# Kernel optimization log

Hardware: AMD Instinct MI355X
Metric: run time of the kernel (lower is better)

Reference implementation:

```python
import jax, jax.numpy as jnp
import numpy as np

N = 40000        # total gene nodes
E = 640000       # edges
F_IN = 128       # num_features
H = 128          # hidden_dim
SUB = 400        # genes per cell
EPS = 1e-5


def _bn(x, g, b):
    # BatchNorm1d, training-mode batch statistics (biased variance), deterministic
    m = x.mean(axis=0)
    v = x.var(axis=0)
    return (x - m) * jax.lax.rsqrt(v + EPS) * g + b


def _gcn_conv(x, W, b, src, dst):
    # PyG GCNConv: h = X W; add self-loops; symmetric deg^{-1/2} normalization;
    # scatter-add messages from src into dst; then add bias.
    h = x @ W                                   # [N, H]
    loop = jnp.arange(N)
    s = jnp.concatenate([src, loop])            # [E+N]
    d = jnp.concatenate([dst, loop])
    deg = jax.ops.segment_sum(jnp.ones(s.shape[0], h.dtype), d, num_segments=N)
    dis = jnp.where(deg > 0, deg ** -0.5, 0.0)  # deg_inv_sqrt
    norm = dis[s] * dis[d]                      # [E+N]
    out = jax.ops.segment_sum(h[s] * norm[:, None], d, num_segments=N)
    return out + b


def setup_inputs() -> dict:
    key = jax.random.key(0)
    ks = jax.random.split(key, 16)
    sc = lambda fan: 1.0 / np.sqrt(fan)
    inp = {
        "x": jax.random.normal(ks[0], (N, F_IN), jnp.float32),
        "edge_index": jax.random.randint(ks[1], (2, E), 0, N, jnp.int64),
        "conv1_w": jax.random.normal(ks[2], (F_IN, H), jnp.float32) * sc(F_IN),
        "conv1_b": jnp.zeros((H,), jnp.float32),
        "bn1_g": jnp.ones((H,), jnp.float32),
        "bn1_b": jnp.zeros((H,), jnp.float32),
        "conv2_w": jax.random.normal(ks[3], (H, H), jnp.float32) * sc(H),
        "conv2_b": jnp.zeros((H,), jnp.float32),
        "bn2_g": jnp.ones((H,), jnp.float32),
        "bn2_b": jnp.zeros((H,), jnp.float32),
        "att_w1": jax.random.normal(ks[4], (H, H // 2), jnp.float32) * sc(H),
        "att_b1": jnp.zeros((H // 2,), jnp.float32),
        "att_w2": jax.random.normal(ks[5], (H // 2, 1), jnp.float32) * sc(H // 2),
        "att_b2": jnp.zeros((1,), jnp.float32),
        "fc_w": jax.random.normal(ks[6], (H, H), jnp.float32) * sc(H),
        "fc_b": jnp.zeros((H,), jnp.float32),
        "bne_g": jnp.ones((H,), jnp.float32),
        "bne_b": jnp.zeros((H,), jnp.float32),
        "bot_w": jax.random.normal(ks[7], (H, 32), jnp.float32) * sc(H),
        "bot_b": jnp.zeros((32,), jnp.float32),
        "bnb_g": jnp.ones((32,), jnp.float32),
        "bnb_b": jnp.zeros((32,), jnp.float32),
    }
    return inp


def reference(x, edge_index, conv1_w, conv1_b, bn1_g, bn1_b,
              conv2_w, conv2_b, bn2_g, bn2_b,
              att_w1, att_b1, att_w2, att_b2,
              fc_w, fc_b, bne_g, bne_b,
              bot_w, bot_b, bnb_g, bnb_b):
    src, dst = edge_index[0], edge_index[1]
    # embed: two GCNConv + BN + ReLU (dropout omitted: deterministic reference)
    h = jax.nn.relu(_bn(_gcn_conv(x, conv1_w, conv1_b, src, dst), bn1_g, bn1_b))
    emb = jax.nn.relu(_bn(_gcn_conv(h, conv2_w, conv2_b, src, dst), bn2_g, bn2_b))
    # attention pooling over genes within each cell
    num_cells = N // SUB
    xr = emb.reshape(num_cells, SUB, H)                      # [C, S, H]
    scores = jnp.tanh(xr @ att_w1 + att_b1) @ att_w2 + att_b2  # [C, S, 1]
    w = jax.nn.softmax(scores, axis=1)
    pooled = jnp.sum(xr * w, axis=1)                          # [C, H]
    # dense head
    y = jax.nn.relu(_bn(pooled @ fc_w + fc_b, bne_g, bne_b))
    y = jax.nn.relu(_bn(y @ bot_w + bot_b, bnb_g, bnb_b))     # [C, 32]
    return (y, emb)
```

## Files before the change

### kernel.cpp

```cpp
#include <hip/hip_runtime.h>
#include <math.h>

typedef unsigned int u32;
typedef __attribute__((ext_vector_type(8))) short bf16x8;
typedef __attribute__((ext_vector_type(4))) float f32x4;

#define NN   40000
#define EE   640000
#define SUBG 400
#define CELLS 100
#define BNEPS 1e-5f
#define GB    2048
#define GEMMB 625
#define DEGB  512
#define FILLB 1024
#define SCALEB 2500

__device__ __forceinline__ u32 bf16pair(float a, float b) {
    u32 ua = __float_as_uint(a), ub = __float_as_uint(b);
    ua += 0x7fffu + ((ua >> 16) & 1u);
    ub += 0x7fffu + ((ub >> 16) & 1u);
    return (ua >> 16) | (ub & 0xffff0000u);
}
__device__ __forceinline__ float bflo(u32 u) { return __uint_as_float(u << 16); }
__device__ __forceinline__ float bfhi(u32 u) { return __uint_as_float(u & 0xffff0000u); }

__global__ void k_init(int* deg_cursor, const float* W1, u32* Wt1,
                       const float* W2, u32* Wt2, const float* wa, u32* Wta,
                       float* hstats) {
    int i = blockIdx.x * 256 + threadIdx.x;
    if (i < 2 * NN) { deg_cursor[i] = 0; return; }
    i -= 2 * NN;
    if (i < 16384) {
        const float* W = (i < 8192) ? W1 : W2;
        u32* Wt = (i < 8192) ? Wt1 : Wt2;
        int j = i & 8191;
        int n = j >> 6, k2 = (j & 63) * 2;
        Wt[n * 64 + (j & 63)] = bf16pair(W[k2 * 128 + n], W[(k2 + 1) * 128 + n]);
        return;
    }
    i -= 16384;
    if (i < 4096) {
        int n = i >> 6, k2 = (i & 63) * 2;
        Wta[n * 64 + (i & 63)] = bf16pair(wa[k2 * 64 + n], wa[(k2 + 1) * 64 + n]);
        return;
    }
    i -= 4096;
    if (i < 320) hstats[i] = 0.f;
}

__global__ __launch_bounds__(256)
void k_gemmdeg(const float* __restrict__ X, const u32* __restrict__ Wt,
               u32* __restrict__ Yb, const int* __restrict__ dst,
               int* __restrict__ deg) {
    int bid = blockIdx.x;
    int t = threadIdx.x;
    if (bid >= GEMMB) {
        int i = (bid - GEMMB) * 256 + t;
        int stride = DEGB * 256;
        for (; i < EE; i += stride) atomicAdd(&deg[dst[i]], 1);
        return;
    }
    int l = t & 63, wv = t >> 6;
    int rowbase = bid * 64 + wv * 16;
    int ml = l & 15, kg = l >> 4;

    f32x4 acc[8];
#pragma unroll
    for (int nt = 0; nt < 8; ++nt) acc[nt] = (f32x4){0.f, 0.f, 0.f, 0.f};
    const float* xr = X + (long)(rowbase + ml) * 128;
#pragma unroll
    for (int kk = 0; kk < 4; ++kk) {
        int k0 = kk * 32 + kg * 8;
        float4 xa = *(const float4*)&xr[k0];
        float4 xb = *(const float4*)&xr[k0 + 4];
        union { u32 u[4]; bf16x8 v; } af;
        af.u[0] = bf16pair(xa.x, xa.y);
        af.u[1] = bf16pair(xa.z, xa.w);
        af.u[2] = bf16pair(xb.x, xb.y);
        af.u[3] = bf16pair(xb.z, xb.w);
#pragma unroll
        for (int nt = 0; nt < 8; ++nt) {
            bf16x8 b = *(const bf16x8*)&Wt[(nt * 16 + ml) * 64 + (k0 >> 1)];
            acc[nt] = __builtin_amdgcn_mfma_f32_16x16x32_bf16(af.v, b, acc[nt], 0, 0, 0);
        }
    }
#pragma unroll
    for (int r = 0; r < 4; ++r) {
        int m = rowbase + kg * 4 + r;
        long obase = (long)m * 64;
#pragma unroll
        for (int nt = 0; nt < 8; ++nt) {
            float v = acc[nt][r];
            float v2 = __shfl_xor(v, 1);
            if ((l & 1) == 0)
                Yb[obase + nt * 8 + (ml >> 1)] = bf16pair(v, v2);
        }
    }
}

__global__ __launch_bounds__(1024)
void k_scan(const int* __restrict__ deg, int* __restrict__ rowstart,
            float* __restrict__ dis) {
    __shared__ int ps[1024];
    int t = threadIdx.x;
    const int4* d4 = (const int4*)deg;
    int sum = 0;
#pragma unroll
    for (int j = 0; j < 10; ++j) {
        int i4 = t * 10 + j;
        if (i4 < 10000) {
            int4 v = d4[i4];
            sum += v.x + v.y + v.z + v.w;
        }
    }
    ps[t] = sum;
    __syncthreads();
    for (int off = 1; off < 1024; off <<= 1) {
        int add = (t >= off) ? ps[t - off] : 0;
        __syncthreads();
        ps[t] += add;
        __syncthreads();
    }
    int run = ps[t] - sum;
#pragma unroll
    for (int j = 0; j < 10; ++j) {
        int i4 = t * 10 + j;
        if (i4 < 10000) {
            int4 v = d4[i4];
            int4 r;
            r.x = run;
            r.y = run + v.x;
            r.z = r.y + v.y;
            r.w = r.z + v.z;
            run = r.w + v.w;
            *(int4*)&rowstart[i4 * 4] = r;
            float4 dv;
            dv.x = rsqrtf((float)(v.x + 1));
            dv.y = rsqrtf((float)(v.y + 1));
            dv.z = rsqrtf((float)(v.z + 1));
            dv.w = rsqrtf((float)(v.w + 1));
            *(float4*)&dis[i4 * 4] = dv;
        }
    }
    if (t == 0) rowstart[NN] = EE;
}

__global__ __launch_bounds__(256)
void k_fillscale(const int* __restrict__ src, const int* __restrict__ dst,
                 const int* __restrict__ rowstart, int* __restrict__ cursor,
                 int* __restrict__ csr_src, uint4* __restrict__ Hb,
                 const float* __restrict__ dis) {
    int bid = blockIdx.x;
    int t = threadIdx.x;
    if (bid < FILLB) {
        int i = bid * 256 + t;
        int stride = FILLB * 256;
        for (; i < EE; i += stride) {
            int d = dst[i];
            int slot = rowstart[d] + atomicAdd(&cursor[d], 1);
            csr_src[slot] = src[i];
        }
        return;
    }
    int i = (bid - FILLB) * 256 + t;
    float dd = dis[i >> 4];
    uint4 v = Hb[i];
    v.x = bf16pair(bflo(v.x) * dd, bfhi(v.x) * dd);
    v.y = bf16pair(bflo(v.y) * dd, bfhi(v.y) * dd);
    v.z = bf16pair(bflo(v.z) * dd, bfhi(v.z) * dd);
    v.w = bf16pair(bflo(v.w) * dd, bfhi(v.w) * dd);
    Hb[i] = v;
}

__global__ __launch_bounds__(256)
void k_gemm_bf16(const u32* __restrict__ Xb, const u32* __restrict__ Wt,
                 u32* __restrict__ Yb, const float* __restrict__ ss,
                 const float* __restrict__ dis) {
    int t = threadIdx.x;
    int l = t & 63, wv = t >> 6;
    int rowbase = blockIdx.x * 64 + wv * 16;
    int ml = l & 15, kg = l >> 4;

    f32x4 acc[8];
#pragma unroll
    for (int nt = 0; nt < 8; ++nt) acc[nt] = (f32x4){0.f, 0.f, 0.f, 0.f};
    const u32* xr = Xb + (long)(rowbase + ml) * 64;
#pragma unroll
    for (int kk = 0; kk < 4; ++kk) {
        int k0 = kk * 32 + kg * 8;
        uint4 xw = *(const uint4*)&xr[k0 >> 1];
        float f0 = bflo(xw.x), f1 = bfhi(xw.x), f2 = bflo(xw.y), f3 = bfhi(xw.y);
        float f4 = bflo(xw.z), f5 = bfhi(xw.z), f6 = bflo(xw.w), f7 = bfhi(xw.w);
        float4 sca = *(const float4*)&ss[k0];
        float4 sha = *(const float4*)&ss[128 + k0];
        float4 scb = *(const float4*)&ss[k0 + 4];
        float4 shb = *(const float4*)&ss[128 + k0 + 4];
        f0 = fmaxf(fmaf(f0, sca.x, sha.x), 0.f);
        f1 = fmaxf(fmaf(f1, sca.y, sha.y), 0.f);
        f2 = fmaxf(fmaf(f2, sca.z, sha.z), 0.f);
        f3 = fmaxf(fmaf(f3, sca.w, sha.w), 0.f);
        f4 = fmaxf(fmaf(f4, scb.x, shb.x), 0.f);
        f5 = fmaxf(fmaf(f5, scb.y, shb.y), 0.f);
        f6 = fmaxf(fmaf(f6, scb.z, shb.z), 0.f);
        f7 = fmaxf(fmaf(f7, scb.w, shb.w), 0.f);
        union { u32 u[4]; bf16x8 v; } af;
        af.u[0] = bf16pair(f0, f1);
        af.u[1] = bf16pair(f2, f3);
        af.u[2] = bf16pair(f4, f5);
        af.u[3] = bf16pair(f6, f7);
#pragma unroll
        for (int nt = 0; nt < 8; ++nt) {
            bf16x8 b = *(const bf16x8*)&Wt[(nt * 16 + ml) * 64 + (k0 >> 1)];
            acc[nt] = __builtin_amdgcn_mfma_f32_16x16x32_bf16(af.v, b, acc[nt], 0, 0, 0);
        }
    }
#pragma unroll
    for (int r = 0; r < 4; ++r) {
        int m = rowbase + kg * 4 + r;
        float dd = dis[m];
        long obase = (long)m * 64;
#pragma unroll
        for (int nt = 0; nt < 8; ++nt) {
            float v = acc[nt][r] * dd;
            float v2 = __shfl_xor(v, 1);
            if ((l & 1) == 0)
                Yb[obase + nt * 8 + (ml >> 1)] = bf16pair(v, v2);
        }
    }
}

__global__ __launch_bounds__(256)
void k_gather_stats(const uint4* __restrict__ Hb, const int* __restrict__ rowstart,
                    const int* __restrict__ csr_src, const float* __restrict__ dis,
                    const float* __restrict__ bias, u32* __restrict__ F1b,
                    float* __restrict__ part) {
    __shared__ float ls[1024], lq[1024];
    int t = threadIdx.x;
    int lane = t & 63, wv = t >> 6;
    int gw = blockIdx.x * 4 + wv;
    int g = lane >> 4, p = lane & 15;
    int c0 = p * 8 + g * 2;
    float2 bb = *(const float2*)&bias[c0];
    float s0 = 0.f, s1 = 0.f, q0 = 0.f, q1 = 0.f;

    for (int node = gw; node < NN; node += GB * 4) {
        float a0 = 0.f, a1 = 0.f, a2 = 0.f, a3 = 0.f, a4 = 0.f, a5 = 0.f, a6 = 0.f, a7 = 0.f;
        if (g == 0) {
            uint4 h = Hb[node * 16 + p];
            a0 = bflo(h.x); a1 = bfhi(h.x);
            a2 = bflo(h.y); a3 = bfhi(h.y);
            a4 = bflo(h.z); a5 = bfhi(h.z);
            a6 = bflo(h.w); a7 = bfhi(h.w);
        }
        int e1 = rowstart[node + 1];
        int e = rowstart[node] + g;
        for (; e + 4 < e1; e += 8) {
            int sA = csr_src[e];
            int sB = csr_src[e + 4];
            uint4 h0 = Hb[sA * 16 + p];
            uint4 h1 = Hb[sB * 16 + p];
            a0 += bflo(h0.x); a1 += bfhi(h0.x);
            a2 += bflo(h0.y); a3 += bfhi(h0.y);
            a4 += bflo(h0.z); a5 += bfhi(h0.z);
            a6 += bflo(h0.w); a7 += bfhi(h0.w);
            a0 += bflo(h1.x); a1 += bfhi(h1.x);
            a2 += bflo(h1.y); a3 += bfhi(h1.y);
            a4 += bflo(h1.z); a5 += bfhi(h1.z);
            a6 += bflo(h1.w); a7 += bfhi(h1.w);
        }
        if (e < e1) {
            int sA = csr_src[e];
            uint4 h0 = Hb[sA * 16 + p];
            a0 += bflo(h0.x); a1 += bfhi(h0.x);
            a2 += bflo(h0.y); a3 += bfhi(h0.y);
            a4 += bflo(h0.z); a5 += bfhi(h0.z);
            a6 += bflo(h0.w); a7 += bfhi(h0.w);
        }
#pragma unroll
        for (int m = 16; m <= 32; m <<= 1) {
            a0 += __shfl_xor(a0, m); a1 += __shfl_xor(a1, m);
            a2 += __shfl_xor(a2, m); a3 += __shfl_xor(a3, m);
            a4 += __shfl_xor(a4, m); a5 += __shfl_xor(a5, m);
            a6 += __shfl_xor(a6, m); a7 += __shfl_xor(a7, m);
        }
        float dd = dis[node];
        float x = (g == 0) ? a0 : (g == 1) ? a2 : (g == 2) ? a4 : a6;
        float y = (g == 0) ? a1 : (g == 1) ? a3 : (g == 2) ? a5 : a7;
        x = fmaf(x, dd, bb.x);
        y = fmaf(y, dd, bb.y);
        u32 pw = bf16pair(x, y);
        F1b[node * 64 + (c0 >> 1)] = pw;
        float rx = bflo(pw), ry = bfhi(pw);
        s0 += rx; s1 += ry; q0 += rx * rx; q1 += ry * ry;
    }
    ls[wv * 128 + c0] = s0; ls[wv * 128 + c0 + 1] = s1;
    lq[wv * 128 + c0] = q0; lq[wv * 128 + c0 + 1] = q1;
    __syncthreads();
    if (t < 128) {
        float S = ls[t] + ls[128 + t] + ls[256 + t] + ls[384 + t];
        float Q = lq[t] + lq[128 + t] + lq[256 + t] + lq[384 + t];
        part[blockIdx.x * 256 + t] = S;
        part[blockIdx.x * 256 + 128 + t] = Q;
    }
}

__global__ __launch_bounds__(256)
void k_bnfinalw(const float* __restrict__ part, const float* __restrict__ g,
                const float* __restrict__ b, float* __restrict__ ss) {
    __shared__ float rs[256], rq[256];
    int c = blockIdx.x, t = threadIdx.x;
    float s = 0.f, q = 0.f;
    for (int i = t; i < GB; i += 256) {
        s += part[i * 256 + c];
        q += part[i * 256 + 128 + c];
    }
    rs[t] = s; rq[t] = q;
    __syncthreads();
    for (int off = 128; off > 0; off >>= 1) {
        if (t < off) { rs[t] += rs[t + off]; rq[t] += rq[t + off]; }
        __syncthreads();
    }
    if (t == 0) {
        float mean = rs[0] * (1.0f / NN);
        float var  = rq[0] * (1.0f / NN) - mean * mean;
        float sc = g[c] * rsqrtf(var + BNEPS);
        ss[c] = sc;
        ss[128 + c] = b[c] - mean * sc;
    }
}

__global__ __launch_bounds__(256)
void k_scoremb(const u32* __restrict__ F1b, const float* __restrict__ ss,
               float* __restrict__ emb,
               const u32* __restrict__ Wta, const float* __restrict__ b1,
               const float* __restrict__ w2, const float* __restrict__ b2,
               float* __restrict__ scores) {
    int t = threadIdx.x;
    int l = t & 63, wv = t >> 6;
    int rowbase = blockIdx.x * 64 + wv * 16;
    int ml = l & 15, kg = l >> 4;

    f32x4 acc[4];
#pragma unroll
    for (int nt = 0; nt < 4; ++nt) acc[nt] = (f32x4){0.f, 0.f, 0.f, 0.f};
    const u32* xr = F1b + (long)(rowbase + ml) * 64;
    float* er = emb + (long)(rowbase + ml) * 128;
#pragma unroll
    for (int kk = 0; kk < 4; ++kk) {
        int k0 = kk * 32 + kg * 8;
        uint4 xw = *(const uint4*)&xr[k0 >> 1];
        float f0 = bflo(xw.x), f1 = bfhi(xw.x), f2 = bflo(xw.y), f3 = bfhi(xw.y);
        float f4 = bflo(xw.z), f5 = bfhi(xw.z), f6 = bflo(xw.w), f7 = bfhi(xw.w);
        float4 sca = *(const float4*)&ss[k0];
        float4 sha = *(const float4*)&ss[128 + k0];
        float4 scb = *(const float4*)&ss[k0 + 4];
        float4 shb = *(const float4*)&ss[128 + k0 + 4];
        f0 = fmaxf(fmaf(f0, sca.x, sha.x), 0.f);
        f1 = fmaxf(fmaf(f1, sca.y, sha.y), 0.f);
        f2 = fmaxf(fmaf(f2, sca.z, sha.z), 0.f);
        f3 = fmaxf(fmaf(f3, sca.w, sha.w), 0.f);
        f4 = fmaxf(fmaf(f4, scb.x, shb.x), 0.f);
        f5 = fmaxf(fmaf(f5, scb.y, shb.y), 0.f);
        f6 = fmaxf(fmaf(f6, scb.z, shb.z), 0.f);
        f7 = fmaxf(fmaf(f7, scb.w, shb.w), 0.f);
        float4 e0 = { f0, f1, f2, f3 };
        float4 e1 = { f4, f5, f6, f7 };
        *(float4*)&er[k0] = e0;
        *(float4*)&er[k0 + 4] = e1;
        union { u32 u[4]; bf16x8 v; } af;
        af.u[0] = bf16pair(f0, f1);
        af.u[1] = bf16pair(f2, f3);
        af.u[2] = bf16pair(f4, f5);
        af.u[3] = bf16pair(f6, f7);
#pragma unroll
        for (int nt = 0; nt < 4; ++nt) {
            bf16x8 b = *(const bf16x8*)&Wta[(nt * 16 + ml) * 64 + (k0 >> 1)];
            acc[nt] = __builtin_amdgcn_mfma_f32_16x16x32_bf16(af.v, b, acc[nt], 0, 0, 0);
        }
    }
    float b1v[4], w2v[4];
#pragma unroll
    for (int nt = 0; nt < 4; ++nt) {
        b1v[nt] = b1[nt * 16 + ml];
        w2v[nt] = w2[nt * 16 + ml];
    }
    float b2v = b2[0];
#pragma unroll
    for (int r = 0; r < 4; ++r) {
        float s = tanhf(acc[0][r] + b1v[0]) * w2v[0]
                + tanhf(acc[1][r] + b1v[1]) * w2v[1]
                + tanhf(acc[2][r] + b1v[2]) * w2v[2]
                + tanhf(acc[3][r] + b1v[3]) * w2v[3];
        s += __shfl_xor(s, 1);
        s += __shfl_xor(s, 2);
        s += __shfl_xor(s, 4);
        s += __shfl_xor(s, 8);
        if (ml == 0) scores[rowbase + kg * 4 + r] = s + b2v;
    }
}

__global__ __launch_bounds__(256)
void k_pool4(const u32* __restrict__ F1b, const float* __restrict__ ss,
             const float* __restrict__ scores, float* __restrict__ pp) {
    __shared__ float sl[SUBG];
    __shared__ float red[256];
    __shared__ float rbuf[512];
    int b = blockIdx.x;
    int c = b >> 2, q = b & 3;
    int t = threadIdx.x;
    int base = c * SUBG;

    float lmax = -1e30f;
    for (int i = t; i < SUBG; i += 256) {
        float v = scores[base + i];
        sl[i] = v;
        lmax = fmaxf(lmax, v);
    }
    red[t] = lmax;
    __syncthreads();
    for (int off = 128; off > 0; off >>= 1) {
        if (t < off) red[t] = fmaxf(red[t], red[t + off]);
        __syncthreads();
    }
    float mx = red[0];
    __syncthreads();
    float lsum = 0.f;
    for (int i = t; i < SUBG; i += 256) {
        float e = __expf(sl[i] - mx);
        sl[i] = e;
        lsum += e;
    }
    red[t] = lsum;
    __syncthreads();
    for (int off = 128; off > 0; off >>= 1) {
        if (t < off) red[t] += red[t + off];
        __syncthreads();
    }
    float inv = 1.0f / red[0];
    __syncthreads();

    int cc = t & 63, gp = t >> 6;
    float2 scv = *(const float2*)&ss[2 * cc];
    float2 shv = *(const float2*)&ss[128 + 2 * cc];
    int g0 = q * 100 + gp * 25;
    float a0 = 0.f, a1 = 0.f;
#pragma unroll 5
    for (int j = 0; j < 25; ++j) {
        int gg = g0 + j;
        u32 v = F1b[(long)(base + gg) * 64 + cc];
        float w = sl[gg] * inv;
        float x0 = fmaxf(fmaf(bflo(v), scv.x, shv.x), 0.f);
        float x1 = fmaxf(fmaf(bfhi(v), scv.y, shv.y), 0.f);
        a0 += w * x0;
        a1 += w * x1;
    }
    rbuf[gp * 128 + 2 * cc] = a0;
    rbuf[gp * 128 + 2 * cc + 1] = a1;
    __syncthreads();
    if (t < 128)
        pp[b * 128 + t] = rbuf[t] + rbuf[128 + t] + rbuf[256 + t] + rbuf[384 + t];
}

__global__ __launch_bounds__(128)
void k_head1r(const float* __restrict__ pp, const float* __restrict__ fc_w,
              const float* __restrict__ fc_b, float* __restrict__ y1pre,
              float* __restrict__ hstats) {
    __shared__ float pr[128];
    int c = blockIdx.x, t = threadIdx.x;
    pr[t] = pp[(c * 4 + 0) * 128 + t] + pp[(c * 4 + 1) * 128 + t]
          + pp[(c * 4 + 2) * 128 + t] + pp[(c * 4 + 3) * 128 + t];
    __syncthreads();
    float a1 = fc_b[t];
#pragma unroll 4
    for (int k = 0; k < 128; ++k) a1 = fmaf(pr[k], fc_w[k * 128 + t], a1);
    y1pre[c * 128 + t] = a1;
    atomicAdd(&hstats[t], a1);
    atomicAdd(&hstats[128 + t], a1 * a1);
}

__global__ __launch_bounds__(128)
void k_head2s(const float* __restrict__ y1pre, const float* __restrict__ hstats,
              const float* __restrict__ bne_g, const float* __restrict__ bne_b,
              const float* __restrict__ bot_w, const float* __restrict__ bot_b,
              float* __restrict__ y2pre, float* __restrict__ hstats2) {
    __shared__ float row[128];
    int c = blockIdx.x, t = threadIdx.x;
    float s = hstats[t], q = hstats[128 + t];
    float mean = s * 0.01f, var = q * 0.01f - mean * mean;
    float scv = bne_g[t] * rsqrtf(var + BNEPS);
    float shv = bne_b[t] - mean * scv;
    row[t] = fmaxf(fmaf(y1pre[c * 128 + t], scv, shv), 0.f);
    __syncthreads();
    if (t < 32) {
        float a2 = bot_b[t];
#pragma unroll 4
        for (int k = 0; k < 128; ++k) a2 = fmaf(row[k], bot_w[k * 32 + t], a2);
        y2pre[c * 32 + t] = a2;
        atomicAdd(&hstats2[t], a2);
        atomicAdd(&hstats2[32 + t], a2 * a2);
    }
}

__global__ __launch_bounds__(256)
void k_out(const float* __restrict__ y2pre, const float* __restrict__ hstats2,
           const float* __restrict__ bnb_g, const float* __restrict__ bnb_b,
           float* __restrict__ y_out) {
    __shared__ float scv[32], shv[32];
    int t = threadIdx.x;
    if (t < 32) {
        float s = hstats2[t], q = hstats2[32 + t];
        float mean = s * 0.01f, var = q * 0.01f - mean * mean;
        float v = bnb_g[t] * rsqrtf(var + BNEPS);
        scv[t] = v; shv[t] = bnb_b[t] - mean * v;
    }
    __syncthreads();
    for (int i = t; i < CELLS * 32; i += 256)
        y_out[i] = fmaxf(fmaf(y2pre[i], scv[i & 31], shv[i & 31]), 0.f);
}

extern "C" void kernel_launch(void* const* d_in, const int* in_sizes, int n_in,
                              void* d_out, int out_size, void* d_ws, size_t ws_size,
                              hipStream_t stream) {
    const float* x        = (const float*)d_in[0];
    const int*   ei       = (const int*)d_in[1];
    const float* conv1_w  = (const float*)d_in[2];
    const float* conv1_b  = (const float*)d_in[3];
    const float* bn1_g    = (const float*)d_in[4];
    const float* bn1_b    = (const float*)d_in[5];
    const float* conv2_w  = (const float*)d_in[6];
    const float* conv2_b  = (const float*)d_in[7];
    const float* bn2_g    = (const float*)d_in[8];
    const float* bn2_b    = (const float*)d_in[9];
    const float* att_w1   = (const float*)d_in[10];
    const float* att_b1   = (const float*)d_in[11];
    const float* att_w2   = (const float*)d_in[12];
    const float* att_b2   = (const float*)d_in[13];
    const float* fc_w     = (const float*)d_in[14];
    const float* fc_b     = (const float*)d_in[15];
    const float* bne_g    = (const float*)d_in[16];
    const float* bne_b    = (const float*)d_in[17];
    const float* bot_w    = (const float*)d_in[18];
    const float* bot_b    = (const float*)d_in[19];
    const float* bnb_g    = (const float*)d_in[20];
    const float* bnb_b    = (const float*)d_in[21];

    const int* src = ei;
    const int* dst = ei + EE;

    float* y_out   = (float*)d_out;
    float* emb_out = y_out + CELLS * 32;

    float* ws = (float*)d_ws;
    u32*   Hb     = (u32*)ws;
    u32*   F1b    = Hb + (long)NN * 64;
    float* dis    = (float*)(F1b + (long)NN * 64);
    float* part   = dis + NN;
    float* ss     = part + GB * 256;
    float* hstats = ss + 256;
    float* y1pre  = hstats + 320;
    float* y2pre  = y1pre + CELLS * 128;
    float* scores = y2pre + CELLS * 32;
    float* pp     = scores + NN;
    u32*   Wt1    = (u32*)(pp + 400 * 128);
    u32*   Wt2    = Wt1 + 8192;
    u32*   Wta    = Wt2 + 8192;
    int*   deg    = (int*)(Wta + 4096);
    int*   cursor = deg + NN;
    int*   rowstart = cursor + NN;
    int*   csr_src  = rowstart + NN + 1;

    k_init<<<394, 256, 0, stream>>>(deg, conv1_w, Wt1, conv2_w, Wt2, att_w1, Wta, hstats);
    k_gemmdeg<<<GEMMB + DEGB, 256, 0, stream>>>(x, Wt1, Hb, dst, deg);
    k_scan<<<1, 1024, 0, stream>>>(deg, rowstart, dis);
    k_fillscale<<<FILLB + SCALEB, 256, 0, stream>>>(src, dst, rowstart, cursor,
                                                    csr_src, (uint4*)Hb, dis);
    k_gather_stats<<<GB, 256, 0, stream>>>((const uint4*)Hb, rowstart, csr_src, dis,
                                           conv1_b, F1b, part);
    k_bnfinalw<<<128, 256, 0, stream>>>(part, bn1_g, bn1_b, ss);
    k_gemm_bf16<<<GEMMB, 256, 0, stream>>>(F1b, Wt2, Hb, ss, dis);
    k_gather_stats<<<GB, 256, 0, stream>>>((const uint4*)Hb, rowstart, csr_src, dis,
                                           conv2_b, F1b, part);
    k_bnfinalw<<<128, 256, 0, stream>>>(part, bn2_g, bn2_b, ss);
    k_scoremb<<<GEMMB, 256, 0, stream>>>(F1b, ss, emb_out, Wta, att_b1, att_w2,
                                         att_b2, scores);
    k_pool4<<<4 * CELLS, 256, 0, stream>>>(F1b, ss, scores, pp);
    k_head1r<<<CELLS, 128, 0, stream>>>(pp, fc_w, fc_b, y1pre, hstats);
    k_head2s<<<CELLS, 128, 0, stream>>>(y1pre, hstats, bne_g, bne_b, bot_w, bot_b,
                                        y2pre, hstats + 256);
    k_out<<<1, 256, 0, stream>>>(y2pre, hstats + 256, bnb_g, bnb_b, y_out);
}
```

Measured before the change: 235.6 us.

## Fuse first GEMM with CSR fill and dis scaling; pack CSR indices as u16

The first X·W1 GEMM moves out of the degree-count kernel and now runs alongside the CSR fill, after the scan. That way it can multiply each row by deg^{-1/2} in its epilogue, which removes the separate read-modify-write scaling pass over Hb. CSR source indices are stored as 16-bit values, since N is below 65536, which halves index traffic in both gather passes. Degree counting becomes a standalone kernel with twice as many blocks. The trade-off is that the GEMM no longer overlaps the atomic degree count, and the u16 packing depends on N staying under 65536.

```diff
diff --git a/kernel.cpp b/kernel.cpp
--- a/kernel.cpp
+++ b/kernel.cpp
@@ -2,6 +2,7 @@
 #include <math.h>
 
 typedef unsigned int u32;
+typedef unsigned short u16;
 typedef __attribute__((ext_vector_type(8))) short bf16x8;
 typedef __attribute__((ext_vector_type(4))) float f32x4;
 
@@ -12,9 +13,8 @@
 #define BNEPS 1e-5f
 #define GB    2048
 #define GEMMB 625
-#define DEGB  512
+#define DEGB  1024
 #define FILLB 1024
-#define SCALEB 2500
 
 __device__ __forceinline__ u32 bf16pair(float a, float b) {
     u32 ua = __float_as_uint(a), ub = __float_as_uint(b);
@@ -49,54 +49,10 @@
     if (i < 320) hstats[i] = 0.f;
 }
 
-__global__ __launch_bounds__(256)
-void k_gemmdeg(const float* __restrict__ X, const u32* __restrict__ Wt,
-               u32* __restrict__ Yb, const int* __restrict__ dst,
-               int* __restrict__ deg) {
-    int bid = blockIdx.x;
-    int t = threadIdx.x;
-    if (bid >= GEMMB) {
-        int i = (bid - GEMMB) * 256 + t;
-        int stride = DEGB * 256;
-        for (; i < EE; i += stride) atomicAdd(&deg[dst[i]], 1);
-        return;
-    }
-    int l = t & 63, wv = t >> 6;
-    int rowbase = bid * 64 + wv * 16;
-    int ml = l & 15, kg = l >> 4;
-
-    f32x4 acc[8];
-#pragma unroll
-    for (int nt = 0; nt < 8; ++nt) acc[nt] = (f32x4){0.f, 0.f, 0.f, 0.f};
-    const float* xr = X + (long)(rowbase + ml) * 128;
-#pragma unroll
-    for (int kk = 0; kk < 4; ++kk) {
-        int k0 = kk * 32 + kg * 8;
-        float4 xa = *(const float4*)&xr[k0];
-        float4 xb = *(const float4*)&xr[k0 + 4];
-        union { u32 u[4]; bf16x8 v; } af;
-        af.u[0] = bf16pair(xa.x, xa.y);
-        af.u[1] = bf16pair(xa.z, xa.w);
-        af.u[2] = bf16pair(xb.x, xb.y);
-        af.u[3] = bf16pair(xb.z, xb.w);
-#pragma unroll
-        for (int nt = 0; nt < 8; ++nt) {
-            bf16x8 b = *(const bf16x8*)&Wt[(nt * 16 + ml) * 64 + (k0 >> 1)];
-            acc[nt] = __builtin_amdgcn_mfma_f32_16x16x32_bf16(af.v, b, acc[nt], 0, 0, 0);
-        }
-    }
-#pragma unroll
-    for (int r = 0; r < 4; ++r) {
-        int m = rowbase + kg * 4 + r;
-        long obase = (long)m * 64;
-#pragma unroll
-        for (int nt = 0; nt < 8; ++nt) {
-            float v = acc[nt][r];
-            float v2 = __shfl_xor(v, 1);
-            if ((l & 1) == 0)
-                Yb[obase + nt * 8 + (ml >> 1)] = bf16pair(v, v2);
-        }
-    }
+__global__ void k_degcount(const int* __restrict__ dst, int* __restrict__ deg) {
+    int i = blockIdx.x * blockDim.x + threadIdx.x;
+    int stride = DEGB * 256;
+    for (; i < EE; i += stride) atomicAdd(&deg[dst[i]], 1);
 }
 
 __global__ __launch_bounds__(1024)
@@ -147,10 +103,11 @@
 }
 
 __global__ __launch_bounds__(256)
-void k_fillscale(const int* __restrict__ src, const int* __restrict__ dst,
-                 const int* __restrict__ rowstart, int* __restrict__ cursor,
-                 int* __restrict__ csr_src, uint4* __restrict__ Hb,
-                 const float* __restrict__ dis) {
+void k_fillgemm(const int* __restrict__ src, const int* __restrict__ dst,
+                const int* __restrict__ rowstart, int* __restrict__ cursor,
+                u16* __restrict__ csr16,
+                const float* __restrict__ X, const u32* __restrict__ Wt,
+                u32* __restrict__ Yb, const float* __restrict__ dis) {
     int bid = blockIdx.x;
     int t = threadIdx.x;
     if (bid < FILLB) {
@@ -159,18 +116,47 @@
         for (; i < EE; i += stride) {
             int d = dst[i];
             int slot = rowstart[d] + atomicAdd(&cursor[d], 1);
-            csr_src[slot] = src[i];
+            csr16[slot] = (u16)src[i];
         }
         return;
     }
-    int i = (bid - FILLB) * 256 + t;
-    float dd = dis[i >> 4];
-    uint4 v = Hb[i];
-    v.x = bf16pair(bflo(v.x) * dd, bfhi(v.x) * dd);
-    v.y = bf16pair(bflo(v.y) * dd, bfhi(v.y) * dd);
-    v.z = bf16pair(bflo(v.z) * dd, bfhi(v.z) * dd);
-    v.w = bf16pair(bflo(v.w) * dd, bfhi(v.w) * dd);
-    Hb[i] = v;
+    int l = t & 63, wv = t >> 6;
+    int rowbase = (bid - FILLB) * 64 + wv * 16;
+    int ml = l & 15, kg = l >> 4;
+
+    f32x4 acc[8];
+#pragma unroll
+    for (int nt = 0; nt < 8; ++nt) acc[nt] = (f32x4){0.f, 0.f, 0.f, 0.f};
+    const float* xr = X + (long)(rowbase + ml) * 128;
+#pragma unroll
+    for (int kk = 0; kk < 4; ++kk) {
+        int k0 = kk * 32 + kg * 8;
+        float4 xa = *(const float4*)&xr[k0];
+        float4 xb = *(const float4*)&xr[k0 + 4];
+        union { u32 u[4]; bf16x8 v; } af;
+        af.u[0] = bf16pair(xa.x, xa.y);
+        af.u[1] = bf16pair(xa.z, xa.w);
+        af.u[2] = bf16pair(xb.x, xb.y);
+        af.u[3] = bf16pair(xb.z, xb.w);
+#pragma unroll
+        for (int nt = 0; nt < 8; ++nt) {
+            bf16x8 b = *(const bf16x8*)&Wt[(nt * 16 + ml) * 64 + (k0 >> 1)];
+            acc[nt] = __builtin_amdgcn_mfma_f32_16x16x32_bf16(af.v, b, acc[nt], 0, 0, 0);
+        }
+    }
+#pragma unroll
+    for (int r = 0; r < 4; ++r) {
+        int m = rowbase + kg * 4 + r;
+        float dd = dis[m];
+        long obase = (long)m * 64;
+#pragma unroll
+        for (int nt = 0; nt < 8; ++nt) {
+            float v = acc[nt][r] * dd;
+            float v2 = __shfl_xor(v, 1);
+            if ((l & 1) == 0)
+                Yb[obase + nt * 8 + (ml >> 1)] = bf16pair(v, v2);
+        }
+    }
 }
 
 __global__ __launch_bounds__(256)
@@ -232,7 +218,7 @@
 
 __global__ __launch_bounds__(256)
 void k_gather_stats(const uint4* __restrict__ Hb, const int* __restrict__ rowstart,
-                    const int* __restrict__ csr_src, const float* __restrict__ dis,
+                    const u16* __restrict__ csr16, const float* __restrict__ dis,
                     const float* __restrict__ bias, u32* __restrict__ F1b,
                     float* __restrict__ part) {
     __shared__ float ls[1024], lq[1024];
@@ -256,8 +242,8 @@
         int e1 = rowstart[node + 1];
         int e = rowstart[node] + g;
         for (; e + 4 < e1; e += 8) {
-            int sA = csr_src[e];
-            int sB = csr_src[e + 4];
+            int sA = csr16[e];
+            int sB = csr16[e + 4];
             uint4 h0 = Hb[sA * 16 + p];
             uint4 h1 = Hb[sB * 16 + p];
             a0 += bflo(h0.x); a1 += bfhi(h0.x);
@@ -270,7 +256,7 @@
             a6 += bflo(h1.w); a7 += bfhi(h1.w);
         }
         if (e < e1) {
-            int sA = csr_src[e];
+            int sA = csr16[e];
             uint4 h0 = Hb[sA * 16 + p];
             a0 += bflo(h0.x); a1 += bfhi(h0.x);
             a2 += bflo(h0.y); a3 += bfhi(h0.y);
@@ -568,18 +554,18 @@
     int*   deg    = (int*)(Wta + 4096);
     int*   cursor = deg + NN;
     int*   rowstart = cursor + NN;
-    int*   csr_src  = rowstart + NN + 1;
+    u16*   csr16  = (u16*)(rowstart + NN + 1);
 
     k_init<<<394, 256, 0, stream>>>(deg, conv1_w, Wt1, conv2_w, Wt2, att_w1, Wta, hstats);
-    k_gemmdeg<<<GEMMB + DEGB, 256, 0, stream>>>(x, Wt1, Hb, dst, deg);
+    k_degcount<<<DEGB, 256, 0, stream>>>(dst, deg);
     k_scan<<<1, 1024, 0, stream>>>(deg, rowstart, dis);
-    k_fillscale<<<FILLB + SCALEB, 256, 0, stream>>>(src, dst, rowstart, cursor,
-                                                    csr_src, (uint4*)Hb, dis);
-    k_gather_stats<<<GB, 256, 0, stream>>>((const uint4*)Hb, rowstart, csr_src, dis,
+    k_fillgemm<<<FILLB + GEMMB, 256, 0, stream>>>(src, dst, rowstart, cursor, csr16,
+                                                  x, Wt1, Hb, dis);
+    k_gather_stats<<<GB, 256, 0, stream>>>((const uint4*)Hb, rowstart, csr16, dis,
                                            conv1_b, F1b, part);
     k_bnfinalw<<<128, 256, 0, stream>>>(part, bn1_g, bn1_b, ss);
     k_gemm_bf16<<<GEMMB, 256, 0, stream>>>(F1b, Wt2, Hb, ss, dis);
-    k_gather_stats<<<GB, 256, 0, stream>>>((const uint4*)Hb, rowstart, csr_src, dis,
+    k_gather_stats<<<GB, 256, 0, stream>>>((const uint4*)Hb, rowstart, csr16, dis,
                                            conv2_b, F1b, part);
     k_bnfinalw<<<128, 256, 0, stream>>>(part, bn2_g, bn2_b, ss);
     k_scoremb<<<GEMMB, 256, 0, stream>>>(F1b, ss, emb_out, Wta, att_b1, att_w2,
```

After: 240.1 us. No clear change (+1.9%).
